# Kernel tuning notes

Measured on AMD Instinct MI355X. Metric: run time of the kernel, lower is better.

Reference implementation:

```python
import jax, jax.numpy as jnp
import numpy as np
from jax import lax

V, E, HD, T = 100000, 256, 512, 11
H = HD // 2
B, S = 32, 512
START, STOP = 9, 10
NEG = -10000.0


def _lstm_dir(x, h0, c0, w_ih, w_hh, b_ih, b_hh):
    # x: (time, batch, in). PyTorch gate order i, f, g, o.
    def step(carry, xt):
        h, c = carry
        g = xt @ w_ih.T + b_ih + h @ w_hh.T + b_hh
        i, f, gg, o = jnp.split(g, 4, axis=-1)
        c = jax.nn.sigmoid(f) * c + jax.nn.sigmoid(i) * jnp.tanh(gg)
        h = jax.nn.sigmoid(o) * jnp.tanh(c)
        return (h, c), h
    _, hs = lax.scan(step, (h0, c0), x)
    return hs


def _features(sentence, embed, w_ih_f, w_hh_f, b_ih_f, b_hh_f,
              w_ih_b, w_hh_b, b_ih_b, b_hh_b, h0, c0, w_out, b_out):
    x = embed[sentence]  # (B, S, E)
    # Faithful to original: torch LSTM is seq-first, so it scans over axis 0 (B)
    # with 'batch' dim S (init_hidden uses sentence.shape[1]).
    hf = _lstm_dir(x, h0[0], c0[0], w_ih_f, w_hh_f, b_ih_f, b_hh_f)
    hb = _lstm_dir(x[::-1], h0[1], c0[1], w_ih_b, w_hh_b, b_ih_b, b_hh_b)[::-1]
    out = jnp.concatenate([hf, hb], axis=-1)  # (B, S, HD)
    return out @ w_out.T + b_out  # (B, S, T)


def _viterbi(feats, transitions):
    # feats: (B, S, T); CRF treats dim0 as batch, dim1 as time (as in source).
    delta0 = jnp.full((feats.shape[0], T), NEG, feats.dtype).at[:, START].set(0.0)

    def step(delta, feat_t):
        sc = transitions[None, :, :] + delta[:, None, :]  # (B, T_to, T_from)
        new = sc.max(-1) + feat_t
        return new, jnp.argmax(sc, -1)

    feats_t = jnp.moveaxis(feats[:, 1:], 1, 0)  # (S-1, B, T)
    deltaT, psis = lax.scan(step, delta0, feats_t)
    score = deltaT.max(-1)            # (B,)
    last = jnp.argmax(deltaT, -1)     # (B,)

    def back(nxt, psi_t):
        tag = jnp.take_along_axis(psi_t, nxt[:, None], axis=-1)[:, 0]
        return tag, tag

    _, earlier = lax.scan(back, last, psis, reverse=True)  # (S-1, B)
    path = jnp.concatenate([earlier, last[None, :]], axis=0).T  # (B, S)
    return score, path


def setup_inputs() -> dict:
    key = jax.random.key(0)
    ks = jax.random.split(key, 20)
    sc = 0.05
    sentence = jax.random.randint(ks[0], (B, S), 0, V)
    embed = jax.random.normal(ks[1], (V, E), jnp.float32) * sc
    w_ih_f = jax.random.normal(ks[2], (4 * H, E), jnp.float32) * sc
    w_hh_f = jax.random.normal(ks[3], (4 * H, H), jnp.float32) * sc
    b_ih_f = jax.random.normal(ks[4], (4 * H,), jnp.float32) * sc
    b_hh_f = jax.random.normal(ks[5], (4 * H,), jnp.float32) * sc
    w_ih_b = jax.random.normal(ks[6], (4 * H, E), jnp.float32) * sc
    w_hh_b = jax.random.normal(ks[7], (4 * H, H), jnp.float32) * sc
    b_ih_b = jax.random.normal(ks[8], (4 * H,), jnp.float32) * sc
    b_hh_b = jax.random.normal(ks[9], (4 * H,), jnp.float32) * sc
    h0 = jax.random.normal(ks[10], (2, S, H), jnp.float32)
    c0 = jax.random.normal(ks[11], (2, S, H), jnp.float32)
    w_out = jax.random.normal(ks[12], (T, HD), jnp.float32) * sc
    b_out = jax.random.normal(ks[13], (T,), jnp.float32) * sc
    transitions = jax.random.normal(ks[14], (T, T), jnp.float32)
    transitions = transitions.at[START, :].set(NEG).at[:, STOP].set(NEG)
    return dict(sentence=sentence, embed=embed,
                w_ih_f=w_ih_f, w_hh_f=w_hh_f, b_ih_f=b_ih_f, b_hh_f=b_hh_f,
                w_ih_b=w_ih_b, w_hh_b=w_hh_b, b_ih_b=b_ih_b, b_hh_b=b_hh_b,
                h0=h0, c0=c0, w_out=w_out, b_out=b_out, transitions=transitions)


def reference(sentence, embed, w_ih_f, w_hh_f, b_ih_f, b_hh_f,
              w_ih_b, w_hh_b, b_ih_b, b_hh_b, h0, c0, w_out, b_out, transitions):
    feats = _features(sentence, embed, w_ih_f, w_hh_f, b_ih_f, b_hh_f,
                      w_ih_b, w_hh_b, b_ih_b, b_hh_b, h0, c0, w_out, b_out)
    return _viterbi(feats, transitions)
```

## Files before the change

kernel.cpp:

```cpp
#include <hip/hip_runtime.h>
#include <math.h>


namespace {

constexpr int T_ = 11;
constexpr int HT = 256 * 512;

__device__ __forceinline__ size_t gq_off(int t, int d, int j, int q, int s) {
  return ((((size_t)(t * 2 + d) * 256 + j) * 4 + q) * 512 + s);
}

__global__ __launch_bounds__(256) void k_prep(
    const float* __restrict__ w_ih_f, const float* __restrict__ w_ih_b,
    const float* __restrict__ w_hh_f, const float* __restrict__ w_hh_b,
    const float* __restrict__ b_ih_f, const float* __restrict__ b_hh_f,
    const float* __restrict__ b_ih_b, const float* __restrict__ b_hh_b,
    const float* __restrict__ h0, const float* __restrict__ c0,
    const float* __restrict__ w_out,
    float* __restrict__ wiq, float* __restrict__ wt4, float* __restrict__ bq,
    float* __restrict__ ct, float* __restrict__ ht_f, float* __restrict__ ht_b,
    float* __restrict__ wot) {
  const int i = blockIdx.x * 256 + threadIdx.x;
  if (i < 524288) {
    int d = i >> 18, r = i & 262143, gcr = r >> 8, k = r & 255;
    int q = gcr >> 8, j = gcr & 255;
    const float* w = d ? w_ih_b : w_ih_f;
    wiq[((size_t)(d * 256 + k) * 256 + j) * 4 + q] = w[gcr * 256 + k];
  } else if (i < 1048576) {
    int i2 = i - 524288;
    int d = i2 >> 18, r = i2 & 262143, gcr = r >> 8, k = r & 255;
    int q = gcr >> 8, j = gcr & 255;
    const float* w = d ? w_hh_b : w_hh_f;
    wt4[((size_t)(d * 256 + k) * 256 + j) * 4 + q] = w[gcr * 256 + k];
  } else if (i < 1050624) {
    int r = i - 1048576;
    int d = r >> 10, x = r & 1023, j = x >> 2, q = x & 3;
    const float* bi = d ? b_ih_b : b_ih_f;
    const float* bh = d ? b_hh_b : b_hh_f;
    bq[r] = bi[q * 256 + j] + bh[q * 256 + j];
  } else if (i < 1312768) {
    int r = i - 1050624;
    int d = r >> 17, y = r & 131071, j = y >> 9, s = y & 511;
    ct[r] = c0[((size_t)d * 512 + s) * 256 + j];
  } else if (i < 1574912) {
    int r = i - 1312768;
    int d = r >> 17, y = r & 131071, j = y >> 9, s = y & 511;
    float v = h0[((size_t)d * 512 + s) * 256 + j];
    if (d == 0) ht_f[y] = v; else ht_b[y] = v;
  } else if (i < 1580544) {
    int r = i - 1574912;
    int k = r / 11, tag = r - k * 11;
    wot[r] = w_out[tag * 512 + k];
  }
}

__global__ __launch_bounds__(256) void k_gatherT(
    const int* __restrict__ sent, const float* __restrict__ embed,
    float* __restrict__ xT) {
  __shared__ float tile[64][65];
  const int bid = blockIdx.x, tid = threadIdx.x;
  const int st = bid & 7, et = (bid >> 3) & 3, t = bid >> 5;
  {
    const int sl = tid >> 2, eq = tid & 3;
    const int tok = sent[t * 512 + st * 64 + sl];
    const float* ep = embed + (size_t)tok * 256 + et * 64 + eq * 16;
    float4 v0 = *(const float4*)(ep);
    float4 v1 = *(const float4*)(ep + 4);
    float4 v2 = *(const float4*)(ep + 8);
    float4 v3 = *(const float4*)(ep + 12);
    const int e0 = eq * 16;
    tile[e0 + 0][sl] = v0.x;  tile[e0 + 1][sl] = v0.y;  tile[e0 + 2][sl] = v0.z;  tile[e0 + 3][sl] = v0.w;
    tile[e0 + 4][sl] = v1.x;  tile[e0 + 5][sl] = v1.y;  tile[e0 + 6][sl] = v1.z;  tile[e0 + 7][sl] = v1.w;
    tile[e0 + 8][sl] = v2.x;  tile[e0 + 9][sl] = v2.y;  tile[e0 + 10][sl] = v2.z; tile[e0 + 11][sl] = v2.w;
    tile[e0 + 12][sl] = v3.x; tile[e0 + 13][sl] = v3.y; tile[e0 + 14][sl] = v3.z; tile[e0 + 15][sl] = v3.w;
  }
  __syncthreads();
  {
    const int el = tid >> 2, sq2 = tid & 3;
    float* op = xT + ((size_t)t * 256 + et * 64 + el) * 512 + st * 64 + sq2 * 16;
    const float* tp = &tile[el][sq2 * 16];
    *(float4*)(op + 0) = make_float4(tp[0], tp[1], tp[2], tp[3]);
    *(float4*)(op + 4) = make_float4(tp[4], tp[5], tp[6], tp[7]);
    *(float4*)(op + 8) = make_float4(tp[8], tp[9], tp[10], tp[11]);
    *(float4*)(op + 12) = make_float4(tp[12], tp[13], tp[14], tp[15]);
  }
}

__global__ __launch_bounds__(512, 4) void k_ggemm(
    const float* __restrict__ xT, const float* __restrict__ wiq,
    const float* __restrict__ bq, float* __restrict__ Gq) {
  const int tid = threadIdx.x, bid = blockIdx.x;
  const int sg = bid & 3, jsl = (bid >> 2) & 15;
  const int d = (bid >> 6) & 1, t = bid >> 7;
  const int wid = __builtin_amdgcn_readfirstlane(tid >> 6);
  const int lane = tid & 63;
  const int jl = lane >> 2, q = lane & 3;
  const int j = jsl * 16 + jl;
  const int s0 = sg * 128 + wid * 16;

  const float* wp = wiq + (size_t)d * 262144 + jsl * 64 + lane;
  const float* xp = xT + (size_t)t * 131072 + s0;

  float acc[16];
#pragma unroll
  for (int i = 0; i < 16; ++i) acc[i] = 0.f;

#pragma unroll 4
  for (int k = 0; k < 256; ++k) {
    const float w = wp[(size_t)k * 1024];
    const float* h = xp + (size_t)k * 512;
    float4 h0_ = *(const float4*)(h);
    float4 h1_ = *(const float4*)(h + 4);
    float4 h2_ = *(const float4*)(h + 8);
    float4 h3_ = *(const float4*)(h + 12);
    acc[0]  = fmaf(w, h0_.x, acc[0]);
    acc[1]  = fmaf(w, h0_.y, acc[1]);
    acc[2]  = fmaf(w, h0_.z, acc[2]);
    acc[3]  = fmaf(w, h0_.w, acc[3]);
    acc[4]  = fmaf(w, h1_.x, acc[4]);
    acc[5]  = fmaf(w, h1_.y, acc[5]);
    acc[6]  = fmaf(w, h1_.z, acc[6]);
    acc[7]  = fmaf(w, h1_.w, acc[7]);
    acc[8]  = fmaf(w, h2_.x, acc[8]);
    acc[9]  = fmaf(w, h2_.y, acc[9]);
    acc[10] = fmaf(w, h2_.z, acc[10]);
    acc[11] = fmaf(w, h2_.w, acc[11]);
    acc[12] = fmaf(w, h3_.x, acc[12]);
    acc[13] = fmaf(w, h3_.y, acc[13]);
    acc[14] = fmaf(w, h3_.z, acc[14]);
    acc[15] = fmaf(w, h3_.w, acc[15]);
  }

  const float bias = bq[(size_t)d * 1024 + jsl * 64 + lane];
  float* op = Gq + gq_off(t, d, j, q, s0);
  *(float4*)(op + 0) = make_float4(acc[0] + bias, acc[1] + bias, acc[2] + bias, acc[3] + bias);
  *(float4*)(op + 4) = make_float4(acc[4] + bias, acc[5] + bias, acc[6] + bias, acc[7] + bias);
  *(float4*)(op + 8) = make_float4(acc[8] + bias, acc[9] + bias, acc[10] + bias, acc[11] + bias);
  *(float4*)(op + 12) = make_float4(acc[12] + bias, acc[13] + bias, acc[14] + bias, acc[15] + bias);
}

__global__ __launch_bounds__(512, 4) void k_rstep(
    const float* __restrict__ wt4, const float* __restrict__ Gq,
    float* __restrict__ ht_f, float* __restrict__ ht_b,
    float* __restrict__ ct, int t) {
  __shared__ float red[3][128][17];
  __shared__ float gb[4][16][33];
  const int tid = threadIdx.x;
  const int bid = blockIdx.x;
  const int jsl = bid & 15, d = (bid >> 4) & 1, sg = bid >> 5;
  const int kh = __builtin_amdgcn_readfirstlane(tid >> 7);
  const int sq = __builtin_amdgcn_readfirstlane((tid >> 6) & 1);
  const int rem = tid & 127;
  const int lane = tid & 63;
  const int j0 = jsl * 16;
  const int s0 = sg * 32 + sq * 16;
  const int tt = d ? 31 - t : t;

  float* htX = d ? ht_b : ht_f;
  const float* hprev = htX + (size_t)t * HT;
  const float* wp = wt4 + ((size_t)d * 256 + (size_t)kh * 64) * 1024 + j0 * 4 + lane;
  const float* hp = hprev + (size_t)kh * 64 * 512 + s0;

  float acc[16];
#pragma unroll
  for (int i = 0; i < 16; ++i) acc[i] = 0.f;

#pragma unroll 4
  for (int k = 0; k < 64; ++k) {
    const float w = wp[(size_t)k * 1024];
    const float* h = hp + (size_t)k * 512;
    float4 h0_ = *(const float4*)(h);
    float4 h1_ = *(const float4*)(h + 4);
    float4 h2_ = *(const float4*)(h + 8);
    float4 h3_ = *(const float4*)(h + 12);
    acc[0]  = fmaf(w, h0_.x, acc[0]);
    acc[1]  = fmaf(w, h0_.y, acc[1]);
    acc[2]  = fmaf(w, h0_.z, acc[2]);
    acc[3]  = fmaf(w, h0_.w, acc[3]);
    acc[4]  = fmaf(w, h1_.x, acc[4]);
    acc[5]  = fmaf(w, h1_.y, acc[5]);
    acc[6]  = fmaf(w, h1_.z, acc[6]);
    acc[7]  = fmaf(w, h1_.w, acc[7]);
    acc[8]  = fmaf(w, h2_.x, acc[8]);
    acc[9]  = fmaf(w, h2_.y, acc[9]);
    acc[10] = fmaf(w, h2_.z, acc[10]);
    acc[11] = fmaf(w, h2_.w, acc[11]);
    acc[12] = fmaf(w, h3_.x, acc[12]);
    acc[13] = fmaf(w, h3_.y, acc[13]);
    acc[14] = fmaf(w, h3_.z, acc[14]);
    acc[15] = fmaf(w, h3_.w, acc[15]);
  }

  if (kh > 0) {
#pragma unroll
    for (int i = 0; i < 16; ++i) red[kh - 1][rem][i] = acc[i];
  }
  __syncthreads();
  if (kh == 0) {
    const int jl = lane >> 2, q = lane & 3;
#pragma unroll
    for (int i = 0; i < 16; ++i) {
      float v = acc[i] + red[0][rem][i] + red[1][rem][i] + red[2][rem][i];
      gb[q][jl][sq * 16 + i] = v;
    }
  }
  __syncthreads();

  {
    const int jl2 = tid >> 5, sp = tid & 31;
    const int j = j0 + jl2;
    const int s = sg * 32 + sp;
    const float* gp = Gq + gq_off(tt, d, j, 0, s);
    float gi = gb[0][jl2][sp] + gp[0];
    float gf = gb[1][jl2][sp] + gp[512];
    float gg = gb[2][jl2][sp] + gp[1024];
    float go = gb[3][jl2][sp] + gp[1536];
    float si = 1.f / (1.f + expf(-gi));
    float sf = 1.f / (1.f + expf(-gf));
    float tg = tanhf(gg);
    float so = 1.f / (1.f + expf(-go));
    const size_t coff = ((size_t)d * 256 + j) * 512 + s;
    float cp = ct[coff];
    float cn = sf * cp + si * tg;
    float hn = so * tanhf(cn);
    ct[coff] = cn;
    htX[(size_t)(t + 1) * HT + (size_t)j * 512 + s] = hn;
  }
}

__global__ __launch_bounds__(256) void k_out(
    const float* __restrict__ ht_f, const float* __restrict__ ht_b,
    const float* __restrict__ wot, const float* __restrict__ b_out,
    float* __restrict__ featsT) {
  __shared__ float red[4][11][64];
  const int tid = threadIdx.x;
  const int bid = blockIdx.x;
  const int t = bid >> 3, stile = bid & 7;
  const int wid = __builtin_amdgcn_readfirstlane(tid >> 6);
  const int lane = tid & 63;
  const int s0 = stile * 64;
  const int kg0 = wid * 128;
  const float* src = (wid < 2)
      ? ht_f + (size_t)(t + 1) * HT + (size_t)kg0 * 512
      : ht_b + (size_t)(32 - t) * HT + (size_t)(kg0 - 256) * 512;

  float acc[11];
#pragma unroll
  for (int g = 0; g < 11; ++g) acc[g] = 0.f;
#pragma unroll 4
  for (int kk = 0; kk < 128; ++kk) {
    float a = src[(size_t)kk * 512 + s0 + lane];
    const float* wp = wot + (size_t)(kg0 + kk) * 11;
#pragma unroll
    for (int g = 0; g < 11; ++g) acc[g] = fmaf(a, wp[g], acc[g]);
  }
#pragma unroll
  for (int g = 0; g < 11; ++g) red[wid][g][lane] = acc[g];
  __syncthreads();
  if (wid == 0) {
#pragma unroll
    for (int g = 0; g < 11; ++g) {
      float v = red[0][g][lane] + red[1][g][lane] + red[2][g][lane] +
                red[3][g][lane] + b_out[g];
      featsT[(size_t)g * 16384 + t * 512 + s0 + lane] = v;
    }
  }
}

__global__ __launch_bounds__(128) void k_viterbi(const float* __restrict__ featsT,
                                                 const float* __restrict__ trans,
                                                 float* __restrict__ out) {
  __shared__ float fl[512 * T_];
  __shared__ unsigned char psiL[511 * T_];
  __shared__ unsigned char specL[121 * 47];
  __shared__ unsigned char selL[16];
  __shared__ int lastL;
  __shared__ float scoreL;
  const int b = blockIdx.x, tid = threadIdx.x;
  for (int i = tid; i < 512 * T_; i += 128) {
    int tag = i >> 9, s = i & 511;
    fl[s * T_ + tag] = featsT[(size_t)tag * 16384 + b * 512 + s];
  }
  __syncthreads();

  if (tid < 64) {
    const int lane = tid;
    const int to = (lane < T_) ? lane : 0;
    float tr[T_];
#pragma unroll
    for (int f = 0; f < T_; ++f) tr[f] = trans[to * T_ + f];
    float delta = (lane == 9) ? 0.f : -10000.f;

    for (int s = 1; s < 512; ++s) {
      float fv = fl[s * T_ + to];
      float v0 = tr[0] + __shfl(delta, 0, 64);
      float v1 = tr[1] + __shfl(delta, 1, 64);
      float v2 = tr[2] + __shfl(delta, 2, 64);
      float v3 = tr[3] + __shfl(delta, 3, 64);
      float v4 = tr[4] + __shfl(delta, 4, 64);
      float v5 = tr[5] + __shfl(delta, 5, 64);
      float v6 = tr[6] + __shfl(delta, 6, 64);
      float v7 = tr[7] + __shfl(delta, 7, 64);
      float v8 = tr[8] + __shfl(delta, 8, 64);
      float v9 = tr[9] + __shfl(delta, 9, 64);
      float v10 = tr[10] + __shfl(delta, 10, 64);
      float mA = fmaxf(fmaxf(v0, v1), v2);
      float mB = fmaxf(fmaxf(v3, v4), v5);
      float mC = fmaxf(fmaxf(v6, v7), v8);
      float mD = fmaxf(v9, v10);
      float m = fmaxf(fmaxf(mA, mB), fmaxf(mC, mD));
      delta = m + fv;
      unsigned msk = (v0 == m) ? 1u : 0u;
      msk |= (v1 == m) ? 2u : 0u;
      msk |= (v2 == m) ? 4u : 0u;
      msk |= (v3 == m) ? 8u : 0u;
      msk |= (v4 == m) ? 16u : 0u;
      msk |= (v5 == m) ? 32u : 0u;
      msk |= (v6 == m) ? 64u : 0u;
      msk |= (v7 == m) ? 128u : 0u;
      msk |= (v8 == m) ? 256u : 0u;
      msk |= (v9 == m) ? 512u : 0u;
      msk |= (v10 == m) ? 1024u : 0u;
      int am = __ffs(msk) - 1;
      if (lane < T_) psiL[(s - 1) * T_ + lane] = (unsigned char)am;
    }
    float d0 = __shfl(delta, 0, 64), d1 = __shfl(delta, 1, 64);
    float d2 = __shfl(delta, 2, 64), d3 = __shfl(delta, 3, 64);
    float d4 = __shfl(delta, 4, 64), d5 = __shfl(delta, 5, 64);
    float d6 = __shfl(delta, 6, 64), d7 = __shfl(delta, 7, 64);
    float d8 = __shfl(delta, 8, 64), d9 = __shfl(delta, 9, 64);
    float d10 = __shfl(delta, 10, 64);
    float mA = fmaxf(fmaxf(d0, d1), d2);
    float mB = fmaxf(fmaxf(d3, d4), d5);
    float mC = fmaxf(fmaxf(d6, d7), d8);
    float mD = fmaxf(d9, d10);
    float m = fmaxf(fmaxf(mA, mB), fmaxf(mC, mD));
    unsigned msk = (d0 == m) ? 1u : 0u;
    msk |= (d1 == m) ? 2u : 0u;
    msk |= (d2 == m) ? 4u : 0u;
    msk |= (d3 == m) ? 8u : 0u;
    msk |= (d4 == m) ? 16u : 0u;
    msk |= (d5 == m) ? 32u : 0u;
    msk |= (d6 == m) ? 64u : 0u;
    msk |= (d7 == m) ? 128u : 0u;
    msk |= (d8 == m) ? 256u : 0u;
    msk |= (d9 == m) ? 512u : 0u;
    msk |= (d10 == m) ? 1024u : 0u;
    int am = __ffs(msk) - 1;
    if (lane == 0) { lastL = am; scoreL = m; }
  }
  __syncthreads();

  const int last = lastL;
  if (tid < 121) {
    const int g = tid / 11, tau = tid - g * 11;
    const int khi = 510 - 47 * g;
    const int len = (g < 10) ? 47 : 41;
    int cur = tau;
    unsigned char* sp = &specL[(g * 11 + tau) * 47];
    for (int i = 0; i < len; ++i) {
      cur = psiL[(khi - i) * T_ + cur];
      sp[i] = (unsigned char)cur;
    }
  }
  __syncthreads();
  if (tid == 0) {
    int cur = last;
    for (int g = 0; g < 11; ++g) {
      selL[g] = (unsigned char)cur;
      int len = (g < 10) ? 47 : 41;
      cur = specL[(g * 11 + cur) * 47 + (len - 1)];
    }
    out[b] = scoreL;
    out[32 + (size_t)b * 512 + 511] = (float)last;
  }
  __syncthreads();
  if (tid < 121) {
    const int g = tid / 11, tau = tid - g * 11;
    if (tau == selL[g]) {
      const int khi = 510 - 47 * g;
      const int len = (g < 10) ? 47 : 41;
      float* path = out + 32 + (size_t)b * 512;
      const unsigned char* sp = &specL[(g * 11 + tau) * 47];
      for (int i = 0; i < len; ++i) path[khi - i] = (float)sp[i];
    }
  }
}

}

extern "C" void kernel_launch(void* const* d_in, const int* in_sizes, int n_in,
                              void* d_out, int out_size, void* d_ws, size_t ws_size,
                              hipStream_t stream) {
  const int* sent     = (const int*)d_in[0];
  const float* embed  = (const float*)d_in[1];
  const float* w_ih_f = (const float*)d_in[2];
  const float* w_hh_f = (const float*)d_in[3];
  const float* b_ih_f = (const float*)d_in[4];
  const float* b_hh_f = (const float*)d_in[5];
  const float* w_ih_b = (const float*)d_in[6];
  const float* w_hh_b = (const float*)d_in[7];
  const float* b_ih_b = (const float*)d_in[8];
  const float* b_hh_b = (const float*)d_in[9];
  const float* h0     = (const float*)d_in[10];
  const float* c0     = (const float*)d_in[11];
  const float* w_out  = (const float*)d_in[12];
  const float* b_out  = (const float*)d_in[13];
  const float* trans  = (const float*)d_in[14];

  float* ws = (float*)d_ws;
  float* Gq     = ws;
  float* ht_f   = Gq + 33554432;
  float* ht_b   = ht_f + 4325376;
  float* ct     = ht_b + 4325376;
  float* wiq    = ct + 262144;
  float* wt4    = wiq + 524288;
  float* bq     = wt4 + 524288;
  float* wot    = bq + 2048;
  float* featsT = wot + 5632;
  float* xT = ht_f + HT;

  k_prep<<<6174, 256, 0, stream>>>(w_ih_f, w_ih_b, w_hh_f, w_hh_b,
                                   b_ih_f, b_hh_f, b_ih_b, b_hh_b,
                                   h0, c0, w_out,
                                   wiq, wt4, bq, ct, ht_f, ht_b, wot);
  k_gatherT<<<1024, 256, 0, stream>>>(sent, embed, xT);
  k_ggemm<<<4096, 512, 0, stream>>>(xT, wiq, bq, Gq);
  for (int t = 0; t < 32; ++t)
    k_rstep<<<512, 512, 0, stream>>>(wt4, Gq, ht_f, ht_b, ct, t);
  k_out<<<256, 256, 0, stream>>>(ht_f, ht_b, wot, b_out, featsT);
  k_viterbi<<<32, 128, 0, stream>>>(featsT, trans, (float*)d_out);
}
```

Measured before the change: 805.5 us.

## Stage hidden/input slabs in LDS with split-K GEMMs; pack Viterbi backpointers

```diff
diff --git a/kernel.cpp b/kernel.cpp
--- a/kernel.cpp
+++ b/kernel.cpp
@@ -9,6 +9,10 @@
 
 __device__ __forceinline__ size_t gq_off(int t, int d, int j, int q, int s) {
   return ((((size_t)(t * 2 + d) * 256 + j) * 4 + q) * 512 + s);
+}
+
+__device__ __forceinline__ float rdlane(float v, int l) {
+  return __uint_as_float(__builtin_amdgcn_readlane(__float_as_uint(v), l));
 }
 
 __global__ __launch_bounds__(256) void k_prep(
@@ -90,26 +94,37 @@
 __global__ __launch_bounds__(512, 4) void k_ggemm(
     const float* __restrict__ xT, const float* __restrict__ wiq,
     const float* __restrict__ bq, float* __restrict__ Gq) {
+  __shared__ float hs[256][36];
+  __shared__ float red[3][128][17];
   const int tid = threadIdx.x, bid = blockIdx.x;
-  const int sg = bid & 3, jsl = (bid >> 2) & 15;
-  const int d = (bid >> 6) & 1, t = bid >> 7;
-  const int wid = __builtin_amdgcn_readfirstlane(tid >> 6);
+  const int sg = bid & 15, jsl = (bid >> 4) & 15;
+  const int d = (bid >> 8) & 1, t = bid >> 9;
+  const int kh = __builtin_amdgcn_readfirstlane(tid >> 7);
+  const int sq = __builtin_amdgcn_readfirstlane((tid >> 6) & 1);
+  const int rem = tid & 127;
   const int lane = tid & 63;
-  const int jl = lane >> 2, q = lane & 3;
-  const int j = jsl * 16 + jl;
-  const int s0 = sg * 128 + wid * 16;
-
-  const float* wp = wiq + (size_t)d * 262144 + jsl * 64 + lane;
-  const float* xp = xT + (size_t)t * 131072 + s0;
+
+  const float* xslab = xT + (size_t)t * 131072 + sg * 32;
+#pragma unroll
+  for (int it = 0; it < 4; ++it) {
+    int idx = tid + 512 * it;
+    int kk2 = idx >> 3, sf = idx & 7;
+    float4 v = *(const float4*)(xslab + (size_t)kk2 * 512 + sf * 4);
+    *(float4*)&hs[kk2][sf * 4] = v;
+  }
+  __syncthreads();
+
+  const float* wp = wiq + (size_t)d * 262144 + (size_t)kh * 64 * 1024 +
+                    jsl * 64 + lane;
 
   float acc[16];
 #pragma unroll
   for (int i = 0; i < 16; ++i) acc[i] = 0.f;
 
 #pragma unroll 4
-  for (int k = 0; k < 256; ++k) {
+  for (int k = 0; k < 64; ++k) {
     const float w = wp[(size_t)k * 1024];
-    const float* h = xp + (size_t)k * 512;
+    const float* h = &hs[kh * 64 + k][sq * 16];
     float4 h0_ = *(const float4*)(h);
     float4 h1_ = *(const float4*)(h + 4);
     float4 h2_ = *(const float4*)(h + 8);
@@ -132,18 +147,32 @@
     acc[15] = fmaf(w, h3_.w, acc[15]);
   }
 
-  const float bias = bq[(size_t)d * 1024 + jsl * 64 + lane];
-  float* op = Gq + gq_off(t, d, j, q, s0);
-  *(float4*)(op + 0) = make_float4(acc[0] + bias, acc[1] + bias, acc[2] + bias, acc[3] + bias);
-  *(float4*)(op + 4) = make_float4(acc[4] + bias, acc[5] + bias, acc[6] + bias, acc[7] + bias);
-  *(float4*)(op + 8) = make_float4(acc[8] + bias, acc[9] + bias, acc[10] + bias, acc[11] + bias);
-  *(float4*)(op + 12) = make_float4(acc[12] + bias, acc[13] + bias, acc[14] + bias, acc[15] + bias);
+  if (kh > 0) {
+#pragma unroll
+    for (int i = 0; i < 16; ++i) red[kh - 1][rem][i] = acc[i];
+  }
+  __syncthreads();
+  if (kh == 0) {
+    const float bias = bq[(size_t)d * 1024 + jsl * 64 + lane];
+    const int jl = lane >> 2, q = lane & 3;
+    const int j = jsl * 16 + jl;
+    const int s0 = sg * 32 + sq * 16;
+    float* op = Gq + gq_off(t, d, j, q, s0);
+#pragma unroll
+    for (int i = 0; i < 16; ++i)
+      acc[i] += red[0][rem][i] + red[1][rem][i] + red[2][rem][i] + bias;
+    *(float4*)(op + 0)  = make_float4(acc[0], acc[1], acc[2], acc[3]);
+    *(float4*)(op + 4)  = make_float4(acc[4], acc[5], acc[6], acc[7]);
+    *(float4*)(op + 8)  = make_float4(acc[8], acc[9], acc[10], acc[11]);
+    *(float4*)(op + 12) = make_float4(acc[12], acc[13], acc[14], acc[15]);
+  }
 }
 
 __global__ __launch_bounds__(512, 4) void k_rstep(
     const float* __restrict__ wt4, const float* __restrict__ Gq,
     float* __restrict__ ht_f, float* __restrict__ ht_b,
     float* __restrict__ ct, int t) {
+  __shared__ float hs[256][36];
   __shared__ float red[3][128][17];
   __shared__ float gb[4][16][33];
   const int tid = threadIdx.x;
@@ -154,13 +183,20 @@
   const int rem = tid & 127;
   const int lane = tid & 63;
   const int j0 = jsl * 16;
-  const int s0 = sg * 32 + sq * 16;
   const int tt = d ? 31 - t : t;
 
   float* htX = d ? ht_b : ht_f;
-  const float* hprev = htX + (size_t)t * HT;
+  const float* hprev = htX + (size_t)t * HT + sg * 32;
+#pragma unroll
+  for (int it = 0; it < 4; ++it) {
+    int idx = tid + 512 * it;
+    int kk2 = idx >> 3, sf = idx & 7;
+    float4 v = *(const float4*)(hprev + (size_t)kk2 * 512 + sf * 4);
+    *(float4*)&hs[kk2][sf * 4] = v;
+  }
+  __syncthreads();
+
   const float* wp = wt4 + ((size_t)d * 256 + (size_t)kh * 64) * 1024 + j0 * 4 + lane;
-  const float* hp = hprev + (size_t)kh * 64 * 512 + s0;
 
   float acc[16];
 #pragma unroll
@@ -169,7 +205,7 @@
 #pragma unroll 4
   for (int k = 0; k < 64; ++k) {
     const float w = wp[(size_t)k * 1024];
-    const float* h = hp + (size_t)k * 512;
+    const float* h = &hs[kh * 64 + k][sq * 16];
     float4 h0_ = *(const float4*)(h);
     float4 h1_ = *(const float4*)(h + 4);
     float4 h2_ = *(const float4*)(h + 8);
@@ -272,7 +308,7 @@
                                                  const float* __restrict__ trans,
                                                  float* __restrict__ out) {
   __shared__ float fl[512 * T_];
-  __shared__ unsigned char psiL[511 * T_];
+  __shared__ unsigned psiP[128][12];
   __shared__ unsigned char specL[121 * 47];
   __shared__ unsigned char selL[16];
   __shared__ int lastL;
@@ -291,20 +327,21 @@
 #pragma unroll
     for (int f = 0; f < T_; ++f) tr[f] = trans[to * T_ + f];
     float delta = (lane == 9) ? 0.f : -10000.f;
+    unsigned pk = 0;
 
     for (int s = 1; s < 512; ++s) {
       float fv = fl[s * T_ + to];
-      float v0 = tr[0] + __shfl(delta, 0, 64);
-      float v1 = tr[1] + __shfl(delta, 1, 64);
-      float v2 = tr[2] + __shfl(delta, 2, 64);
-      float v3 = tr[3] + __shfl(delta, 3, 64);
-      float v4 = tr[4] + __shfl(delta, 4, 64);
-      float v5 = tr[5] + __shfl(delta, 5, 64);
-      float v6 = tr[6] + __shfl(delta, 6, 64);
-      float v7 = tr[7] + __shfl(delta, 7, 64);
-      float v8 = tr[8] + __shfl(delta, 8, 64);
-      float v9 = tr[9] + __shfl(delta, 9, 64);
-      float v10 = tr[10] + __shfl(delta, 10, 64);
+      float v0 = tr[0] + rdlane(delta, 0);
+      float v1 = tr[1] + rdlane(delta, 1);
+      float v2 = tr[2] + rdlane(delta, 2);
+      float v3 = tr[3] + rdlane(delta, 3);
+      float v4 = tr[4] + rdlane(delta, 4);
+      float v5 = tr[5] + rdlane(delta, 5);
+      float v6 = tr[6] + rdlane(delta, 6);
+      float v7 = tr[7] + rdlane(delta, 7);
+      float v8 = tr[8] + rdlane(delta, 8);
+      float v9 = tr[9] + rdlane(delta, 9);
+      float v10 = tr[10] + rdlane(delta, 10);
       float mA = fmaxf(fmaxf(v0, v1), v2);
       float mB = fmaxf(fmaxf(v3, v4), v5);
       float mC = fmaxf(fmaxf(v6, v7), v8);
@@ -322,15 +359,22 @@
       msk |= (v8 == m) ? 256u : 0u;
       msk |= (v9 == m) ? 512u : 0u;
       msk |= (v10 == m) ? 1024u : 0u;
-      int am = __ffs(msk) - 1;
-      if (lane < T_) psiL[(s - 1) * T_ + lane] = (unsigned char)am;
-    }
-    float d0 = __shfl(delta, 0, 64), d1 = __shfl(delta, 1, 64);
-    float d2 = __shfl(delta, 2, 64), d3 = __shfl(delta, 3, 64);
-    float d4 = __shfl(delta, 4, 64), d5 = __shfl(delta, 5, 64);
-    float d6 = __shfl(delta, 6, 64), d7 = __shfl(delta, 7, 64);
-    float d8 = __shfl(delta, 8, 64), d9 = __shfl(delta, 9, 64);
-    float d10 = __shfl(delta, 10, 64);
+      unsigned am = (unsigned)(__ffs(msk) - 1);
+      const int r = (s - 1) & 3;
+      pk |= am << (r * 8);
+      if (r == 3) {
+        if (lane < T_) psiP[(s - 1) >> 2][lane] = pk;
+        pk = 0;
+      }
+    }
+    if (lane < T_) psiP[127][lane] = pk;
+
+    float d0 = rdlane(delta, 0), d1 = rdlane(delta, 1);
+    float d2 = rdlane(delta, 2), d3 = rdlane(delta, 3);
+    float d4 = rdlane(delta, 4), d5 = rdlane(delta, 5);
+    float d6 = rdlane(delta, 6), d7 = rdlane(delta, 7);
+    float d8 = rdlane(delta, 8), d9 = rdlane(delta, 9);
+    float d10 = rdlane(delta, 10);
     float mA = fmaxf(fmaxf(d0, d1), d2);
     float mB = fmaxf(fmaxf(d3, d4), d5);
     float mC = fmaxf(fmaxf(d6, d7), d8);
@@ -360,7 +404,8 @@
     int cur = tau;
     unsigned char* sp = &specL[(g * 11 + tau) * 47];
     for (int i = 0; i < len; ++i) {
-      cur = psiL[(khi - i) * T_ + cur];
+      const int k = khi - i;
+      cur = (int)((psiP[k >> 2][cur] >> ((k & 3) * 8)) & 0xffu);
       sp[i] = (unsigned char)cur;
     }
   }
@@ -426,7 +471,7 @@
                                    h0, c0, w_out,
                                    wiq, wt4, bq, ct, ht_f, ht_b, wot);
   k_gatherT<<<1024, 256, 0, stream>>>(sent, embed, xT);
-  k_ggemm<<<4096, 512, 0, stream>>>(xT, wiq, bq, Gq);
+  k_ggemm<<<16384, 512, 0, stream>>>(xT, wiq, bq, Gq);
   for (int t = 0; t < 32; ++t)
     k_rstep<<<512, 512, 0, stream>>>(wt4, Gq, ht_f, ht_b, ct, t);
   k_out<<<256, 256, 0, stream>>>(ht_f, ht_b, wot, b_out, featsT);
```

Result: slower. 899.7 us (+11.7%).
